# Kernel tuning notes

Measured on AMD Instinct MI355X. Metric: run time of the kernel, lower is better.

Reference implementation:

```python
import jax, jax.numpy as jnp
import numpy as np

K = 5          # number of neighbors (topk k=5+1, drop self)
EPS = 1e-05    # hparams['epsilon'] for gentropy term


def setup_inputs() -> dict:
    key = jax.random.key(0)
    k1, k2, k3, k4, k5 = jax.random.split(key, 5)
    B, D, C, N = 256, 256, 64, 200000
    features = jax.random.normal(k1, (B, D), dtype=jnp.float32)
    W = jax.random.normal(k2, (D, C), dtype=jnp.float32) * 0.05
    b = jnp.zeros((C,), dtype=jnp.float32)
    fea_bank = jax.random.normal(k3, (N, D), dtype=jnp.float32)
    # score bank holds softmax outputs -> make rows valid probability distributions
    score_bank = jax.nn.softmax(jax.random.normal(k4, (N, C), dtype=jnp.float32), axis=-1)
    trg_idx = jax.random.randint(k5, (B,), 0, N, dtype=jnp.int64)
    return {"features": features, "W": W, "b": b,
            "fea_bank": fea_bank, "score_bank": score_bank, "trg_idx": trg_idx}


def reference(features, W, b, fea_bank, score_bank, trg_idx):
    sg = jax.lax.stop_gradient
    B = features.shape[0]
    C = W.shape[1]

    logits = features @ W + b                       # classifier(features)
    softmax_out = jax.nn.softmax(logits, axis=-1)   # [B, C] (differentiable)

    # --- everything bank-related is under torch.no_grad in the original ---
    nrm = jnp.maximum(jnp.linalg.norm(features, axis=1, keepdims=True), 1e-12)
    f_norm = sg(features / nrm)                     # F.normalize(features)
    fb = sg(fea_bank.at[trg_idx].set(f_norm))        # fea_bank[trg_idx] = f_norm
    sb = sg(score_bank.at[trg_idx].set(sg(softmax_out)))

    dist = f_norm @ fb.T                             # [B, N]
    _, idx_near = jax.lax.top_k(dist, K + 1)
    idx_near = idx_near[:, 1:]                       # [B, K] drop self

    score_near = sb[idx_near]                        # [B, K, C]
    fea_near = fb[idx_near]                          # [B, K, D]

    dist2 = jnp.einsum('bkd,nd->bkn', fea_near, fb)  # [B, K, N]
    _, idx_nn = jax.lax.top_k(dist2, K + 1)
    idx_nn = idx_nn[:, :, 1:]                        # [B, K, K]

    match = (idx_nn == trg_idx[:, None, None]).sum(-1).astype(jnp.float32)  # [B, K]
    weight = jnp.where(match > 0.0, match, jnp.float32(0.1))                # [B, K]
    weight_kk = jnp.full((B, K * K), 0.1, dtype=jnp.float32)  # fill_(0.1) overwrites

    score_near_kk = sb[idx_nn].reshape(B, K * K, C)  # [B, K*K, C]
    # --- end no_grad region ---

    # F.kl_div(input, target, reduction='none') = target * (log(target) - input)
    # (original passes probabilities, not log-probs, as input -- kept faithfully)
    kl_kk = score_near_kk * (jnp.log(score_near_kk) - softmax_out[:, None, :])
    loss = jnp.mean((kl_kk.sum(-1) * weight_kk).sum(1))

    kl_n = score_near * (jnp.log(score_near) - softmax_out[:, None, :])
    loss = loss + jnp.mean((kl_n.sum(-1) * weight).sum(1))

    msoftmax = softmax_out.mean(axis=0)
    gentropy = jnp.sum(msoftmax * jnp.log(msoftmax + EPS))
    loss = loss + gentropy
    return loss
```

## Files before the change

### kernel.cpp

```cpp
#include <hip/hip_runtime.h>
#include <hip/hip_bf16.h>
#include <math.h>

#define B_SZ   256
#define D_DIM  256
#define C_DIM  64
#define N_CAND 200000
#define K_TOP  5
#define CH32   32
#define CH32_SH 8192
#define QTILE_SH 16384
#define NCH32  (N_CAND / CH32)
#define CMSTR  6256
#define NCHJ1  16
#define NCHJ2  32
#define S1     ((NCH32 + NCHJ1 - 1) / NCHJ1)
#define S2     ((NCH32 + NCHJ2 - 1) / NCHJ2)
#define MAXC   192

typedef short bf16x8 __attribute__((ext_vector_type(8)));
typedef float f32x16 __attribute__((ext_vector_type(16)));
typedef unsigned short u16x8 __attribute__((ext_vector_type(8)));

__device__ __forceinline__ bool better(float v1, int i1, float v2, int i2) {
    return (v1 > v2) || (v1 == v2 && i1 < i2);
}

__device__ __forceinline__ void insert6f(float* lv, int* li, float v, int idx) {
    if (better(v, idx, lv[5], li[5])) {
        lv[5] = v; li[5] = idx;
        #pragma unroll
        for (int k = 5; k > 0; --k) {
            if (better(lv[k], li[k], lv[k - 1], li[k - 1])) {
                float tv = lv[k]; lv[k] = lv[k - 1]; lv[k - 1] = tv;
                int   ti = li[k]; li[k] = li[k - 1]; li[k - 1] = ti;
            }
        }
    }
}

__device__ __forceinline__ void merge6(const float* av, const int* ai,
                                       const float* bv, const int* bi,
                                       float* ov, int* oi) {
    int ia = 0, ib = 0;
    #pragma unroll
    for (int k = 0; k < 6; ++k) {
        bool ta;
        if (ia >= 6)      ta = false;
        else if (ib >= 6) ta = true;
        else              ta = better(av[ia], ai[ia], bv[ib], bi[ib]);
        if (ta) { ov[k] = av[ia]; oi[k] = ai[ia]; ++ia; }
        else    { ov[k] = bv[ib]; oi[k] = bi[ib]; ++ib; }
    }
}

__device__ __forceinline__ unsigned short bf16rne(float x) {
    unsigned int u = __float_as_uint(x);
    unsigned int r = u + 0x7fffu + ((u >> 16) & 1u);
    return (unsigned short)(r >> 16);
}

__device__ __forceinline__ float bf16f(unsigned short h) {
    return __uint_as_float(((unsigned)h) << 16);
}

__device__ __forceinline__ u16x8 pack8(float4 a, float4 b) {
    u16x8 h;
    h[0] = bf16rne(a.x); h[1] = bf16rne(a.y); h[2] = bf16rne(a.z); h[3] = bf16rne(a.w);
    h[4] = bf16rne(b.x); h[5] = bf16rne(b.y); h[6] = bf16rne(b.z); h[7] = bf16rne(b.w);
    return h;
}

__global__ void k_init(int* pos_of, float* accp) {
    int i = blockIdx.x * 256 + threadIdx.x;
    if (i < N_CAND) pos_of[i] = -1;
    if (i == 0) accp[0] = 0.f;
}

__global__ void k_scatter(const int* __restrict__ trg, int* __restrict__ pos_of) {
    int j = threadIdx.x;
    atomicMax(&pos_of[trg[j]], j);
}

__global__ __launch_bounds__(256) void k_prep(const float* __restrict__ features,
                                              const float* __restrict__ W,
                                              const float* __restrict__ bias,
                                              float* __restrict__ f_norm,
                                              float* __restrict__ softm) {
    int b = blockIdx.x, t = threadIdx.x;
    __shared__ float row[256];
    __shared__ float red[256];
    float x = features[b * D_DIM + t];
    row[t] = x; red[t] = x * x;
    __syncthreads();
    for (int s = 128; s > 0; s >>= 1) {
        if (t < s) red[t] += red[t + s];
        __syncthreads();
    }
    float nrm = fmaxf(sqrtf(red[0]), 1e-12f);
    f_norm[b * D_DIM + t] = x / nrm;
    if (t < C_DIM) {
        float acc = bias[t];
        for (int d = 0; d < D_DIM; ++d) acc = fmaf(row[d], W[d * C_DIM + t], acc);
        float mx = acc;
        for (int off = 32; off > 0; off >>= 1) mx = fmaxf(mx, __shfl_xor(mx, off, 64));
        float e = expf(acc - mx);
        float ssum = e;
        for (int off = 32; off > 0; off >>= 1) ssum += __shfl_xor(ssum, off, 64);
        softm[b * C_DIM + t] = e / ssum;
    }
}

__global__ __launch_bounds__(256) void k_convert(const float* __restrict__ fea_bank,
                                                 const float* __restrict__ f_norm,
                                                 const int* __restrict__ pos_of,
                                                 short* __restrict__ bank) {
    int cc = blockIdx.x, t = threadIdx.x;
    int r = t >> 2, q4 = t & 3;
    int n = cc * 64 + r;
    int p = pos_of[n];
    const float* src = (p >= 0) ? (f_norm + (size_t)p * D_DIM)
                                : (fea_bank + (size_t)n * D_DIM);
    short* dst = bank + (size_t)(cc * 2 + (r >> 5)) * CH32_SH;
    int rl = r & 31;
    #pragma unroll
    for (int i = 0; i < 8; ++i) {
        int kk = i * 32 + q4 * 8;
        float4 a = *(const float4*)(src + kk);
        float4 b = *(const float4*)(src + kk + 4);
        int e = ((kk >> 4) * 64) + (((kk >> 3) & 1) * 32) + rl;
        *(u16x8*)(dst + (size_t)e * 8) = pack8(a, b);
    }
}

__global__ __launch_bounds__(256) void k_permq(const float* __restrict__ rows,
                                               const float* __restrict__ fea_bank,
                                               const int* __restrict__ idx,
                                               const int* __restrict__ pos_of,
                                               short* __restrict__ dst,
                                               unsigned short* __restrict__ qplain) {
    int tile = blockIdx.x, t = threadIdx.x;
    int r = t >> 2, q4 = t & 3;
    const float* src;
    if (idx) {
        int n = idx[tile * 64 + r];
        int p = pos_of[n];
        src = (p >= 0) ? (rows + (size_t)p * D_DIM) : (fea_bank + (size_t)n * D_DIM);
    } else {
        src = rows + (size_t)(tile * 64 + r) * D_DIM;
    }
    short* d = dst + (size_t)tile * QTILE_SH;
    unsigned short* qp = qplain + (size_t)(tile * 64 + r) * D_DIM;
    #pragma unroll
    for (int i = 0; i < 8; ++i) {
        int kk = i * 32 + q4 * 8;
        float4 a = *(const float4*)(src + kk);
        float4 b = *(const float4*)(src + kk + 4);
        u16x8 h = pack8(a, b);
        int e = ((kk >> 4) * 128) + ((r >> 5) * 64) + (((kk >> 3) & 1) * 32) + (r & 31);
        *(u16x8*)(d + (size_t)e * 8) = h;
        *(u16x8*)(qp + kk) = h;
    }
}

__global__ __launch_bounds__(256, 2)
__attribute__((amdgpu_waves_per_eu(2, 2)))
void dist_max(const short* __restrict__ qbf,
              const short* __restrict__ bank,
              unsigned short* __restrict__ cmax,
              int nqt, int swz,
              int S, int nchj) {
    __shared__ __align__(16) short sbuf[4 * CH32_SH];
    __shared__ unsigned short cmaxbuf[32 * 256];

    int slab, qt;
    if (swz) {
        int bid = blockIdx.x;
        int xcd = bid & 7;
        int rem = bid >> 3;
        qt = rem % nqt;
        slab = (rem / nqt) * 8 + xcd;
        if (slab >= S) return;
    } else {
        slab = blockIdx.x;
        qt = blockIdx.y;
    }
    const int cfirst = slab * nchj;
    int nch = NCH32 - cfirst; if (nch > nchj) nch = nchj;

    const int t   = threadIdx.x;
    const int w   = t >> 6;
    const int l   = t & 63;
    const int khv = l >> 5;
    const int col = l & 31;

    const short* qtile = qbf + (size_t)(qt * 4 + w) * QTILE_SH;
    bf16x8 bfr0[16], bfr1[16];
    #pragma unroll
    for (int ks = 0; ks < 16; ++ks) {
        bfr0[ks] = *(const bf16x8*)(qtile + (size_t)(ks * 128      + l) * 8);
        bfr1[ks] = *(const bf16x8*)(qtile + (size_t)(ks * 128 + 64 + l) * 8);
    }

    const short* sbase = bank + (size_t)cfirst * CH32_SH;

    #pragma unroll
    for (int c = 0; c < 3; ++c) {
        const short* g = sbase + (size_t)c * CH32_SH;
        short* lbase = sbuf + (size_t)c * CH32_SH;
        #pragma unroll
        for (int i = 0; i < 4; ++i) {
            const short* gp = g + (size_t)(i * 256 + t) * 8;
            short* lp = lbase + (size_t)(i * 256 + w * 64) * 8;
            __builtin_amdgcn_global_load_lds(
                (const __attribute__((address_space(1))) void*)gp,
                (__attribute__((address_space(3))) void*)lp, 16, 0, 0);
        }
    }

    for (int ch = 0; ch < nch; ++ch) {
        int ahead = nch - 1 - ch;
        if (ahead >= 2)      asm volatile("s_waitcnt vmcnt(8)" ::: "memory");
        else if (ahead == 1) asm volatile("s_waitcnt vmcnt(4)" ::: "memory");
        else                 asm volatile("s_waitcnt vmcnt(0)" ::: "memory");
        __builtin_amdgcn_s_barrier();
        __builtin_amdgcn_sched_barrier(0);

        const short* cb = sbuf + (size_t)(ch & 3) * CH32_SH;

        f32x16 a0 = {}, a1 = {};
        __builtin_amdgcn_s_setprio(1);
        #pragma unroll
        for (int ks = 0; ks < 16; ++ks) {
            bf16x8 fa = *(const bf16x8*)(cb + (size_t)(ks * 64 + l) * 8);
            a0 = __builtin_amdgcn_mfma_f32_32x32x16_bf16(fa, bfr0[ks], a0, 0, 0, 0);
            a1 = __builtin_amdgcn_mfma_f32_32x32x16_bf16(fa, bfr1[ks], a1, 0, 0, 0);
        }
        __builtin_amdgcn_s_setprio(0);

        float m0 = a0[0], m1 = a1[0];
        #pragma unroll
        for (int r = 1; r < 16; ++r) { m0 = fmaxf(m0, a0[r]); m1 = fmaxf(m1, a1[r]); }
        m0 = fmaxf(m0, __shfl_xor(m0, 32, 64));
        m1 = fmaxf(m1, __shfl_xor(m1, 32, 64));
        if (khv == 0) {
            cmaxbuf[ch * 256 + w * 64 + col]      = bf16rne(m0);
            cmaxbuf[ch * 256 + w * 64 + 32 + col] = bf16rne(m1);
        }

        if (ch + 3 < nch) {
            const short* g = sbase + (size_t)(ch + 3) * CH32_SH;
            short* lbase = sbuf + (size_t)((ch + 3) & 3) * CH32_SH;
            #pragma unroll
            for (int i = 0; i < 4; ++i) {
                const short* gp = g + (size_t)(i * 256 + t) * 8;
                short* lp = lbase + (size_t)(i * 256 + w * 64) * 8;
                __builtin_amdgcn_global_load_lds(
                    (const __attribute__((address_space(1))) void*)gp,
                    (__attribute__((address_space(3))) void*)lp, 16, 0, 0);
            }
        }
    }

    __syncthreads();
    {
        size_t gbase = (size_t)(qt * 256 + t) * CMSTR + cfirst;
        int c0 = 0;
        for (; c0 + 8 <= nch; c0 += 8) {
            u16x8 h;
            #pragma unroll
            for (int i = 0; i < 8; ++i) h[i] = cmaxbuf[(c0 + i) * 256 + t];
            *(u16x8*)(cmax + gbase + c0) = h;
        }
        for (; c0 < nch; ++c0) cmax[gbase + c0] = cmaxbuf[c0 * 256 + t];
        int cend = CMSTR - cfirst; if (cend > nchj) cend = nchj;
        for (int cp = nch; cp < cend; ++cp) cmax[gbase + cp] = 0xFF7F;
    }
}

__global__ __launch_bounds__(256) void k_select(const unsigned short* __restrict__ cmax,
                                                const unsigned short* __restrict__ qplain,
                                                const short* __restrict__ bank,
                                                int* __restrict__ out_idx) {
    int q = blockIdx.x, t = threadIdx.x;
    __shared__ float sv[256][6];
    __shared__ int   si[256][6];
    __shared__ float qrow[256];
    __shared__ int cnt;
    __shared__ int list[MAXC];

    const unsigned short* row = cmax + (size_t)q * CMSTR;

    float lv[6]; int li[6];
    #pragma unroll
    for (int k = 0; k < 6; ++k) { lv[k] = -3.4e38f; li[k] = 0x7fffffff; }
    for (int c0 = t * 8; c0 < CMSTR; c0 += 2048) {
        u16x8 h = *(const u16x8*)(row + c0);
        float m8 = bf16f(h[0]);
        #pragma unroll
        for (int i = 1; i < 8; ++i) m8 = fmaxf(m8, bf16f(h[i]));
        if (better(m8, c0, lv[5], li[5])) {
            #pragma unroll
            for (int i = 0; i < 8; ++i) {
                int c = c0 + i;
                if (c < NCH32) insert6f(lv, li, bf16f(h[i]), c);
            }
        }
    }
    #pragma unroll
    for (int k = 0; k < 6; ++k) { sv[t][k] = lv[k]; si[t][k] = li[k]; }
    if (t == 0) cnt = 0;
    __syncthreads();
    for (int w = 128; w >= 1; w >>= 1) {
        if (t < w) {
            float ov[6]; int oi[6];
            merge6(sv[t], si[t], sv[t + w], si[t + w], ov, oi);
            #pragma unroll
            for (int k = 0; k < 6; ++k) { sv[t][k] = ov[k]; si[t][k] = oi[k]; }
        }
        __syncthreads();
    }
    float tauM = sv[0][5] - 6e-3f;
    __syncthreads();

    for (int c0 = t * 8; c0 < CMSTR; c0 += 2048) {
        u16x8 h = *(const u16x8*)(row + c0);
        float m8 = bf16f(h[0]);
        #pragma unroll
        for (int i = 1; i < 8; ++i) m8 = fmaxf(m8, bf16f(h[i]));
        if (m8 >= tauM) {
            #pragma unroll
            for (int i = 0; i < 8; ++i) {
                int c = c0 + i;
                if (c < NCH32 && bf16f(h[i]) >= tauM) {
                    int k = atomicAdd(&cnt, 1);
                    if (k < MAXC) list[k] = c;
                }
            }
        }
    }
    qrow[t] = bf16f(qplain[(size_t)q * D_DIM + t]);
    __syncthreads();
    int nc = cnt < MAXC ? cnt : MAXC;

    float bv[6]; int bi[6];
    #pragma unroll
    for (int k = 0; k < 6; ++k) { bv[k] = -3.4e38f; bi[k] = 0x7fffffff; }
    const int cand = t >> 3, j = t & 7;
    for (int ci = 0; ci < nc; ++ci) {
        int c = list[ci];
        const short* cb = bank + (size_t)c * CH32_SH;
        u16x8 h0 = *(const u16x8*)(cb + (size_t)(128 * j +  0 + cand) * 8);
        u16x8 h1 = *(const u16x8*)(cb + (size_t)(128 * j + 32 + cand) * 8);
        u16x8 h2 = *(const u16x8*)(cb + (size_t)(128 * j + 64 + cand) * 8);
        u16x8 h3 = *(const u16x8*)(cb + (size_t)(128 * j + 96 + cand) * 8);
        int d0 = j * 32;
        float acc = 0.f;
        #pragma unroll
        for (int d = 0; d < 8; ++d) {
            acc = fmaf(bf16f(h0[d]), qrow[d0 + d], acc);
            acc = fmaf(bf16f(h1[d]), qrow[d0 + 8 + d], acc);
            acc = fmaf(bf16f(h2[d]), qrow[d0 + 16 + d], acc);
            acc = fmaf(bf16f(h3[d]), qrow[d0 + 24 + d], acc);
        }
        acc += __shfl_down(acc, 4, 8);
        acc += __shfl_down(acc, 2, 8);
        acc += __shfl_down(acc, 1, 8);
        if (j == 0) insert6f(bv, bi, acc, c * CH32 + cand);
    }

    #pragma unroll
    for (int k = 0; k < 6; ++k) { sv[t][k] = bv[k]; si[t][k] = bi[k]; }
    __syncthreads();
    for (int w = 128; w >= 1; w >>= 1) {
        if (t < w) {
            float ov[6]; int oi[6];
            merge6(sv[t], si[t], sv[t + w], si[t + w], ov, oi);
            #pragma unroll
            for (int k = 0; k < 6; ++k) { sv[t][k] = ov[k]; si[t][k] = oi[k]; }
        }
        __syncthreads();
    }
    if (t == 0) {
        for (int k = 1; k < 6; ++k) out_idx[q * K_TOP + k - 1] = si[0][k];
    }
}

__global__ void k_loss(const float* __restrict__ softm, const float* __restrict__ score_bank,
                       const int* __restrict__ pos_of, const int* __restrict__ idx_near,
                       const int* __restrict__ idx_nn, const int* __restrict__ trg,
                       float* accp) {
    int b = blockIdx.x, c = threadIdx.x;
    float p_bc = softm[b * C_DIM + c];
    float part = 0.f;
    for (int k = 0; k < K_TOP; ++k) {
        for (int j = 0; j < K_TOP; ++j) {
            int n = idx_nn[(b * K_TOP + k) * K_TOP + j];
            int p = pos_of[n];
            const float* srow = (p >= 0) ? (softm + (size_t)p * C_DIM)
                                         : (score_bank + (size_t)n * C_DIM);
            float s = srow[c];
            float v = s * (logf(s) - p_bc);
            for (int off = 32; off > 0; off >>= 1) v += __shfl_down(v, off, 64);
            if (c == 0) part += 0.1f * v;
        }
    }
    for (int k = 0; k < K_TOP; ++k) {
        int n = idx_near[b * K_TOP + k];
        int p = pos_of[n];
        const float* srow = (p >= 0) ? (softm + (size_t)p * C_DIM)
                                     : (score_bank + (size_t)n * C_DIM);
        float s = srow[c];
        float v = s * (logf(s) - p_bc);
        for (int off = 32; off > 0; off >>= 1) v += __shfl_down(v, off, 64);
        if (c == 0) {
            int m = 0;
            for (int j = 0; j < K_TOP; ++j)
                m += (idx_nn[(b * K_TOP + k) * K_TOP + j] == trg[b]) ? 1 : 0;
            float w = (m > 0) ? (float)m : 0.1f;
            part += w * v;
        }
    }
    if (c == 0) atomicAdd(accp, part * (1.0f / (float)B_SZ));
}

__global__ void k_final(const float* __restrict__ softm, const float* __restrict__ accp,
                        float* __restrict__ out) {
    int c = threadIdx.x;
    float m = 0.f;
    for (int b = 0; b < B_SZ; ++b) m += softm[b * C_DIM + c];
    m *= (1.0f / (float)B_SZ);
    float g = m * logf(m + 1e-5f);
    for (int off = 32; off > 0; off >>= 1) g += __shfl_down(g, off, 64);
    if (c == 0) out[0] = accp[0] + g;
}

extern "C" void kernel_launch(void* const* d_in, const int* in_sizes, int n_in,
                              void* d_out, int out_size, void* d_ws, size_t ws_size,
                              hipStream_t stream) {
    const float* features   = (const float*)d_in[0];
    const float* W          = (const float*)d_in[1];
    const float* bias       = (const float*)d_in[2];
    const float* fea_bank   = (const float*)d_in[3];
    const float* score_bank = (const float*)d_in[4];
    const int*   trg        = (const int*)d_in[5];
    float* out = (float*)d_out;

    char* ws = (char*)d_ws;
    size_t off = 0;
    auto alloc = [&](size_t bytes) -> void* {
        void* p = ws + off;
        off = (off + bytes + 255) & ~(size_t)255;
        return p;
    };
    short* bankbf   = (short*)alloc((size_t)NCH32 * CH32_SH * 2);
    short* q1bf     = (short*)alloc((size_t)(B_SZ / 64) * QTILE_SH * 2);
    short* q2bf     = (short*)alloc((size_t)(B_SZ * K_TOP / 64) * QTILE_SH * 2);
    unsigned short* qplain1 = (unsigned short*)alloc((size_t)B_SZ * D_DIM * 2);
    unsigned short* qplain2 = (unsigned short*)alloc((size_t)B_SZ * K_TOP * D_DIM * 2);
    float* f_norm   = (float*)alloc((size_t)B_SZ * D_DIM * 4);
    float* softm    = (float*)alloc((size_t)B_SZ * C_DIM * 4);
    int*   pos_of   = (int*)alloc((size_t)N_CAND * 4);
    float* accp     = (float*)alloc(4);
    int*   idx_near = (int*)alloc((size_t)B_SZ * K_TOP * 4);
    int*   idx_nn   = (int*)alloc((size_t)B_SZ * K_TOP * K_TOP * 4);
    unsigned short* cmax1 = (unsigned short*)alloc((size_t)B_SZ * CMSTR * 2);
    unsigned short* cmax2 = (unsigned short*)alloc((size_t)B_SZ * K_TOP * CMSTR * 2);

    k_init<<<dim3((N_CAND + 255) / 256), dim3(256), 0, stream>>>(pos_of, accp);
    k_scatter<<<dim3(1), dim3(256), 0, stream>>>(trg, pos_of);
    k_prep<<<dim3(B_SZ), dim3(256), 0, stream>>>(features, W, bias, f_norm, softm);

    k_convert<<<dim3(NCH32 / 2), dim3(256), 0, stream>>>(fea_bank, f_norm, pos_of, bankbf);
    k_permq<<<dim3(B_SZ / 64), dim3(256), 0, stream>>>(
        f_norm, fea_bank, nullptr, pos_of, q1bf, qplain1);

    dist_max<<<dim3(S1, 1), dim3(256), 0, stream>>>(
        q1bf, bankbf, cmax1, 1, 0, S1, NCHJ1);
    k_select<<<dim3(B_SZ), dim3(256), 0, stream>>>(cmax1, qplain1, bankbf, idx_near);

    k_permq<<<dim3(B_SZ * K_TOP / 64), dim3(256), 0, stream>>>(
        f_norm, fea_bank, idx_near, pos_of, q2bf, qplain2);

    {
        int nqt = (B_SZ * K_TOP) / 256;
        int nsg = (S2 + 7) / 8;
        dist_max<<<dim3(nsg * 8 * nqt), dim3(256), 0, stream>>>(
            q2bf, bankbf, cmax2, nqt, 1, S2, NCHJ2);
    }
    k_select<<<dim3(B_SZ * K_TOP), dim3(256), 0, stream>>>(cmax2, qplain2, bankbf, idx_nn);

    k_loss<<<dim3(B_SZ), dim3(64), 0, stream>>>(softm, score_bank, pos_of, idx_near, idx_nn, trg, accp);
    k_final<<<dim3(1), dim3(64), 0, stream>>>(softm, accp, out);
}
```

Measured before the change: 316.9 us.

## Fuse first-pass distance max into bank conversion kernel

The bank fp32-to-bf16 conversion kernel now also stages each 64-row chunk in LDS and runs the first query pass (256 queries) with MFMA on it, writing per-chunk maxima directly. This removes the separate first dist_max launch and its re-read of the converted bank from global memory. Padding of the cmax rows moves into k_permq. The trade-off is more LDS and registers in the convert kernel, which may lower its occupancy, and smaller work per block for the first pass.

```diff
diff --git a/kernel.cpp b/kernel.cpp
--- a/kernel.cpp
+++ b/kernel.cpp
@@ -12,9 +12,7 @@
 #define QTILE_SH 16384
 #define NCH32  (N_CAND / CH32)
 #define CMSTR  6256
-#define NCHJ1  16
 #define NCHJ2  32
-#define S1     ((NCH32 + NCHJ1 - 1) / NCHJ1)
 #define S2     ((NCH32 + NCHJ2 - 1) / NCHJ2)
 #define MAXC   192
 
@@ -111,34 +109,13 @@
     }
 }
 
-__global__ __launch_bounds__(256) void k_convert(const float* __restrict__ fea_bank,
-                                                 const float* __restrict__ f_norm,
-                                                 const int* __restrict__ pos_of,
-                                                 short* __restrict__ bank) {
-    int cc = blockIdx.x, t = threadIdx.x;
-    int r = t >> 2, q4 = t & 3;
-    int n = cc * 64 + r;
-    int p = pos_of[n];
-    const float* src = (p >= 0) ? (f_norm + (size_t)p * D_DIM)
-                                : (fea_bank + (size_t)n * D_DIM);
-    short* dst = bank + (size_t)(cc * 2 + (r >> 5)) * CH32_SH;
-    int rl = r & 31;
-    #pragma unroll
-    for (int i = 0; i < 8; ++i) {
-        int kk = i * 32 + q4 * 8;
-        float4 a = *(const float4*)(src + kk);
-        float4 b = *(const float4*)(src + kk + 4);
-        int e = ((kk >> 4) * 64) + (((kk >> 3) & 1) * 32) + rl;
-        *(u16x8*)(dst + (size_t)e * 8) = pack8(a, b);
-    }
-}
-
 __global__ __launch_bounds__(256) void k_permq(const float* __restrict__ rows,
                                                const float* __restrict__ fea_bank,
                                                const int* __restrict__ idx,
                                                const int* __restrict__ pos_of,
                                                short* __restrict__ dst,
-                                               unsigned short* __restrict__ qplain) {
+                                               unsigned short* __restrict__ qplain,
+                                               unsigned short* __restrict__ cmax_pad) {
     int tile = blockIdx.x, t = threadIdx.x;
     int r = t >> 2, q4 = t & 3;
     const float* src;
@@ -161,6 +138,80 @@
         *(u16x8*)(d + (size_t)e * 8) = h;
         *(u16x8*)(qp + kk) = h;
     }
+    if (t < 64) {
+        size_t base = (size_t)(tile * 64 + t) * CMSTR + NCH32;
+        #pragma unroll
+        for (int k = 0; k < 6; ++k) cmax_pad[base + k] = 0xFF7F;
+    }
+}
+
+__global__ __launch_bounds__(256) void k_convert(const float* __restrict__ fea_bank,
+                                                 const float* __restrict__ f_norm,
+                                                 const int* __restrict__ pos_of,
+                                                 const short* __restrict__ qbf,
+                                                 short* __restrict__ bank,
+                                                 unsigned short* __restrict__ cmax) {
+    __shared__ __align__(16) short ls[2 * CH32_SH];
+    __shared__ unsigned short cmaxbuf[2 * 256];
+
+    int cc = blockIdx.x, t = threadIdx.x;
+    int r = t >> 2, q4 = t & 3;
+    int n = cc * 64 + r;
+    int p = pos_of[n];
+    const float* src = (p >= 0) ? (f_norm + (size_t)p * D_DIM)
+                                : (fea_bank + (size_t)n * D_DIM);
+    short* dst = bank + (size_t)(cc * 2 + (r >> 5)) * CH32_SH;
+    short* lds = ls + (size_t)(r >> 5) * CH32_SH;
+    int rl = r & 31;
+    #pragma unroll
+    for (int i = 0; i < 8; ++i) {
+        int kk = i * 32 + q4 * 8;
+        float4 a = *(const float4*)(src + kk);
+        float4 b = *(const float4*)(src + kk + 4);
+        u16x8 h = pack8(a, b);
+        int e = ((kk >> 4) * 64) + (((kk >> 3) & 1) * 32) + rl;
+        *(u16x8*)(dst + (size_t)e * 8) = h;
+        *(u16x8*)(lds + (size_t)e * 8) = h;
+    }
+
+    const int w   = t >> 6;
+    const int l   = t & 63;
+    const int khv = l >> 5;
+    const int col = l & 31;
+    const short* qtile = qbf + (size_t)w * QTILE_SH;
+    bf16x8 bfr0[16], bfr1[16];
+    #pragma unroll
+    for (int ks = 0; ks < 16; ++ks) {
+        bfr0[ks] = *(const bf16x8*)(qtile + (size_t)(ks * 128      + l) * 8);
+        bfr1[ks] = *(const bf16x8*)(qtile + (size_t)(ks * 128 + 64 + l) * 8);
+    }
+    __syncthreads();
+
+    #pragma unroll
+    for (int ch = 0; ch < 2; ++ch) {
+        const short* cb = ls + (size_t)ch * CH32_SH;
+        f32x16 a0 = {}, a1 = {};
+        #pragma unroll
+        for (int ks = 0; ks < 16; ++ks) {
+            bf16x8 fa = *(const bf16x8*)(cb + (size_t)(ks * 64 + l) * 8);
+            a0 = __builtin_amdgcn_mfma_f32_32x32x16_bf16(fa, bfr0[ks], a0, 0, 0, 0);
+            a1 = __builtin_amdgcn_mfma_f32_32x32x16_bf16(fa, bfr1[ks], a1, 0, 0, 0);
+        }
+        float m0 = a0[0], m1 = a1[0];
+        #pragma unroll
+        for (int rr = 1; rr < 16; ++rr) { m0 = fmaxf(m0, a0[rr]); m1 = fmaxf(m1, a1[rr]); }
+        m0 = fmaxf(m0, __shfl_xor(m0, 32, 64));
+        m1 = fmaxf(m1, __shfl_xor(m1, 32, 64));
+        if (khv == 0) {
+            cmaxbuf[ch * 256 + w * 64 + col]      = bf16rne(m0);
+            cmaxbuf[ch * 256 + w * 64 + 32 + col] = bf16rne(m1);
+        }
+    }
+    __syncthreads();
+    {
+        unsigned v = (unsigned)cmaxbuf[t] | ((unsigned)cmaxbuf[256 + t] << 16);
+        *(unsigned*)&cmax[(size_t)t * CMSTR + cc * 2] = v;
+    }
 }
 
 __global__ __launch_bounds__(256, 2)
@@ -168,23 +219,17 @@
 void dist_max(const short* __restrict__ qbf,
               const short* __restrict__ bank,
               unsigned short* __restrict__ cmax,
-              int nqt, int swz,
-              int S, int nchj) {
+              int nqt, int S, int nchj) {
     __shared__ __align__(16) short sbuf[4 * CH32_SH];
     __shared__ unsigned short cmaxbuf[32 * 256];
 
-    int slab, qt;
-    if (swz) {
-        int bid = blockIdx.x;
-        int xcd = bid & 7;
-        int rem = bid >> 3;
-        qt = rem % nqt;
-        slab = (rem / nqt) * 8 + xcd;
-        if (slab >= S) return;
-    } else {
-        slab = blockIdx.x;
-        qt = blockIdx.y;
-    }
+    int bid = blockIdx.x;
+    int xcd = bid & 7;
+    int rem = bid >> 3;
+    int qt = rem % nqt;
+    int slab = (rem / nqt) * 8 + xcd;
+    if (slab >= S) return;
+
     const int cfirst = slab * nchj;
     int nch = NCH32 - cfirst; if (nch > nchj) nch = nchj;
 
@@ -273,8 +318,6 @@
             *(u16x8*)(cmax + gbase + c0) = h;
         }
         for (; c0 < nch; ++c0) cmax[gbase + c0] = cmaxbuf[c0 * 256 + t];
-        int cend = CMSTR - cfirst; if (cend > nchj) cend = nchj;
-        for (int cp = nch; cp < cend; ++cp) cmax[gbase + cp] = 0xFF7F;
     }
 }
 
@@ -471,22 +514,22 @@
     k_scatter<<<dim3(1), dim3(256), 0, stream>>>(trg, pos_of);
     k_prep<<<dim3(B_SZ), dim3(256), 0, stream>>>(features, W, bias, f_norm, softm);
 
-    k_convert<<<dim3(NCH32 / 2), dim3(256), 0, stream>>>(fea_bank, f_norm, pos_of, bankbf);
     k_permq<<<dim3(B_SZ / 64), dim3(256), 0, stream>>>(
-        f_norm, fea_bank, nullptr, pos_of, q1bf, qplain1);
-
-    dist_max<<<dim3(S1, 1), dim3(256), 0, stream>>>(
-        q1bf, bankbf, cmax1, 1, 0, S1, NCHJ1);
+        f_norm, fea_bank, nullptr, pos_of, q1bf, qplain1, cmax1);
+
+    k_convert<<<dim3(NCH32 / 2), dim3(256), 0, stream>>>(
+        fea_bank, f_norm, pos_of, q1bf, bankbf, cmax1);
+
     k_select<<<dim3(B_SZ), dim3(256), 0, stream>>>(cmax1, qplain1, bankbf, idx_near);
 
     k_permq<<<dim3(B_SZ * K_TOP / 64), dim3(256), 0, stream>>>(
-        f_norm, fea_bank, idx_near, pos_of, q2bf, qplain2);
+        f_norm, fea_bank, idx_near, pos_of, q2bf, qplain2, cmax2);
 
     {
         int nqt = (B_SZ * K_TOP) / 256;
         int nsg = (S2 + 7) / 8;
         dist_max<<<dim3(nsg * 8 * nqt), dim3(256), 0, stream>>>(
-            q2bf, bankbf, cmax2, nqt, 1, S2, NCHJ2);
+            q2bf, bankbf, cmax2, nqt, S2, NCHJ2);
     }
     k_select<<<dim3(B_SZ * K_TOP), dim3(256), 0, stream>>>(cmax2, qplain2, bankbf, idx_nn);
 
```

Measured after the change: 299.7 us. 5.4% less time.
